# Kernel tuning notes

Hardware: AMD Instinct MI355X
Metric: run time of the kernel (lower is better)

Reference implementation:

```python
import jax, jax.numpy as jnp
import numpy as np

TEMP = 8.0      # config.router_temp
TOP_K = 2       # config.moe_top_k
EPS = 1e-8
LN_EPS = 1e-5


def _layer_norm_noaffine(x):
    # nn.LayerNorm(input_dim, elementwise_affine=False)
    mu = jnp.mean(x, axis=-1, keepdims=True)
    var = jnp.var(x, axis=-1, keepdims=True)
    return (x - mu) / jnp.sqrt(var + LN_EPS)


def _unit_norm(x):
    # x / x.norm(dim=-1).clamp(min=EPS)
    n = jnp.linalg.norm(x, axis=-1, keepdims=True)
    return x / jnp.maximum(n, EPS)


def setup_inputs() -> dict:
    key = jax.random.key(0)
    k1, k2 = jax.random.split(key)
    x = jax.random.normal(k1, (4, 4096, 2048), dtype=jnp.float32)
    prototypes = jax.random.normal(k2, (64, 2048), dtype=jnp.float32)
    return {"x": x, "prototypes": prototypes}


def reference(x, prototypes):
    # input_norm_fn = 'norm_d', proto_norm_fn = 'unit'
    xn = _layer_norm_noaffine(x)          # [b, s, d]
    pn = _unit_norm(prototypes)           # [e, d]
    logits = jnp.einsum('bsd,ed->bse', xn, pn) / TEMP   # [b, s, e]
    probs = jax.nn.softmax(logits, axis=-1)
    top_w, top_i = jax.lax.top_k(probs, TOP_K)          # [b, s, k]
    top_w = top_w / jnp.sum(top_w, axis=-1, keepdims=True)
    return top_w, top_i
```

## Files before the change

### kernel.cpp

```cpp
#include <hip/hip_runtime.h>
#include <math.h>

typedef __attribute__((ext_vector_type(8))) short short8;
typedef __attribute__((ext_vector_type(4))) float f32x4;

constexpr int kD  = 2048;
constexpr int kE  = 64;
constexpr int kM  = 16;
constexpr int kBK = 128;
constexpr int kIt = kD / kBK;
constexpr int kCS = 3136;

constexpr int kPlaneU = 4 * 64 * 512;
__device__ unsigned short g_B[3 * kPlaneU];

__device__ __forceinline__ void split3(float v, unsigned& h, unsigned& m, unsigned& l) {
  unsigned u = __float_as_uint(v);
  h = u & 0xFFFF0000u;
  float r1 = v - __uint_as_float(h);
  m = __float_as_uint(r1) & 0xFFFF0000u;
  float r2 = r1 - __uint_as_float(m);
  l = __float_as_uint(r2);
}

__device__ __forceinline__ void pack2(float e0, float e1,
                                      unsigned& dh, unsigned& dm, unsigned& dl) {
  unsigned h0, m0, l0, h1, m1, l1;
  split3(e0, h0, m0, l0);
  split3(e1, h1, m1, l1);
  dh = (h0 >> 16) | h1;
  dm = (m0 >> 16) | m1;
  dl = (l0 >> 16) | (l1 & 0xFFFF0000u);
}

__global__ __launch_bounds__(256) void proto_prep(const float* __restrict__ p,
                                                  float* __restrict__ ws) {
  const int e = blockIdx.x, t = threadIdx.x;
  const float* row = p + (size_t)e * kD;
  float4 v0 = *(const float4*)(row + 8 * t);
  float4 v1 = *(const float4*)(row + 8 * t + 4);

  unsigned dh[4], dm[4], dl[4];
  pack2(v0.x, v0.y, dh[0], dm[0], dl[0]);
  pack2(v0.z, v0.w, dh[1], dm[1], dl[1]);
  pack2(v1.x, v1.y, dh[2], dm[2], dl[2]);
  pack2(v1.z, v1.w, dh[3], dm[3], dl[3]);
  const int gc = t >> 2, o = t & 3;
  size_t base = (size_t)((e >> 4) * 64 + gc) * 512 + (16 * o + (e & 15)) * 8;
  *(uint4*)&g_B[base]               = make_uint4(dh[0], dh[1], dh[2], dh[3]);
  *(uint4*)&g_B[kPlaneU + base]     = make_uint4(dm[0], dm[1], dm[2], dm[3]);
  *(uint4*)&g_B[2 * kPlaneU + base] = make_uint4(dl[0], dl[1], dl[2], dl[3]);

  float s = (v0.x + v0.y) + (v0.z + v0.w) + (v1.x + v1.y) + (v1.z + v1.w);
  float q = v0.x*v0.x + v0.y*v0.y + v0.z*v0.z + v0.w*v0.w
          + v1.x*v1.x + v1.y*v1.y + v1.z*v1.z + v1.w*v1.w;
  #pragma unroll
  for (int off = 32; off >= 1; off >>= 1) {
    s += __shfl_xor(s, off, 64);
    q += __shfl_xor(q, off, 64);
  }
  __shared__ float as[4], aq[4];
  if ((t & 63) == 0) { as[t >> 6] = s; aq[t >> 6] = q; }
  __syncthreads();
  if (t == 0) {
    float S = (as[0] + as[1]) + (as[2] + as[3]);
    float Q = (aq[0] + aq[1]) + (aq[2] + aq[3]);
    ws[e]      = S;
    ws[kE + e] = 1.f / fmaxf(sqrtf(Q), 1e-8f);
  }
}

__global__ __launch_bounds__(256, 4) void router_main(
    const float* __restrict__ x, const float* __restrict__ ws,
    float* __restrict__ out_w, float* __restrict__ out_i) {
  __shared__ __align__(16) unsigned char sA[4 * kCS];
  __shared__ float sLogit[kM * 68];
  __shared__ float sStats[kM][2];

  const int t    = threadIdx.x;
  const int w    = t >> 6;
  const int L    = t & 63;
  const int ln15 = L & 15;
  const int q    = L >> 4;
  const int tok0 = blockIdx.x * kM;
  const float* xg = x + (size_t)tok0 * kD;

  f32x4 acc = (f32x4){0.f, 0.f, 0.f, 0.f};
  float sx[2] = {0.f, 0.f}, sxx[2] = {0.f, 0.f};

  float4 pf[2];
  #pragma unroll
  for (int jj = 0; jj < 2; ++jj) {
    int f = t + 256 * jj;
    pf[jj] = *(const float4*)(xg + (size_t)(f >> 5) * kD + (f & 31) * 4);
  }

  for (int it = 0; it < kIt; ++it) {
    __syncthreads();
    #pragma unroll
    for (int jj = 0; jj < 2; ++jj) {
      int f = t + 256 * jj;
      int c4 = f & 31, k = 4 * c4;
      int m = f >> 5, c = k >> 5, o = (k >> 3) & 3, j = k & 7;
      float4 v = pf[jj];
      sx[jj] += (v.x + v.y) + (v.z + v.w);
      sxx[jj] = fmaf(v.x, v.x, fmaf(v.y, v.y, fmaf(v.z, v.z, fmaf(v.w, v.w, sxx[jj]))));
      unsigned dh0, dm0, dl0, dh1, dm1, dl1;
      pack2(v.x, v.y, dh0, dm0, dl0);
      pack2(v.z, v.w, dh1, dm1, dl1);
      unsigned char* dst = sA + c * kCS + (16 * o + m) * 48 + o * 16 + j * 2;
      *(uint2*)(dst)      = make_uint2(dh0, dh1);
      *(uint2*)(dst + 16) = make_uint2(dm0, dm1);
      *(uint2*)(dst + 32) = make_uint2(dl0, dl1);
    }
    __syncthreads();
    if (it + 1 < kIt) {
      #pragma unroll
      for (int jj = 0; jj < 2; ++jj) {
        int f = t + 256 * jj;
        pf[jj] = *(const float4*)(xg + (size_t)(f >> 5) * kD + (it + 1) * kBK + (f & 31) * 4);
      }
    }
    #pragma unroll
    for (int c = 0; c < 4; ++c) {
      const int gc = it * 4 + c;
      const size_t bo = (size_t)(w * 64 + gc) * 512 + L * 8;
      short8 bh = *(const short8*)&g_B[bo];
      short8 bm = *(const short8*)&g_B[kPlaneU + bo];
      short8 bl = *(const short8*)&g_B[2 * kPlaneU + bo];
      const unsigned char* ra = sA + c * kCS + L * 48 + (L >> 4) * 16;
      short8 ah = *(const short8*)(ra);
      short8 am = *(const short8*)(ra + 16);
      short8 al = *(const short8*)(ra + 32);
      acc = __builtin_amdgcn_mfma_f32_16x16x32_bf16(ah, bh, acc, 0, 0, 0);
      acc = __builtin_amdgcn_mfma_f32_16x16x32_bf16(ah, bm, acc, 0, 0, 0);
      acc = __builtin_amdgcn_mfma_f32_16x16x32_bf16(am, bh, acc, 0, 0, 0);
      acc = __builtin_amdgcn_mfma_f32_16x16x32_bf16(am, bm, acc, 0, 0, 0);
      acc = __builtin_amdgcn_mfma_f32_16x16x32_bf16(ah, bl, acc, 0, 0, 0);
      acc = __builtin_amdgcn_mfma_f32_16x16x32_bf16(al, bh, acc, 0, 0, 0);
    }
  }

  #pragma unroll
  for (int jj = 0; jj < 2; ++jj) {
    float a = sx[jj], b = sxx[jj];
    #pragma unroll
    for (int off = 16; off >= 1; off >>= 1) {
      a += __shfl_xor(a, off, 64);
      b += __shfl_xor(b, off, 64);
    }
    if ((L & 31) == 0) {
      int m = (t >> 5) + 8 * jj;
      sStats[m][0] = a;
      sStats[m][1] = b;
    }
  }

  #pragma unroll
  for (int i = 0; i < 4; ++i)
    sLogit[(q * 4 + i) * 68 + w * 16 + ln15] = acc[i];
  __syncthreads();

  const float Se  = ws[L];
  const float inv = ws[kE + L];
  #pragma unroll
  for (int tl = 0; tl < 4; ++tl) {
    int tk = w * 4 + tl;
    float mu   = sStats[tk][0] * (1.f / kD);
    float var  = sStats[tk][1] * (1.f / kD) - mu * mu;
    float rstd = rsqrtf(var + 1e-5f);
    float logit = (sLogit[tk * 68 + L] - mu * Se) * rstd * inv * 0.125f;

    float v1 = logit; int i1 = L;
    #pragma unroll
    for (int off = 32; off >= 1; off >>= 1) {
      float ov = __shfl_xor(v1, off, 64);
      int   oi = __shfl_xor(i1, off, 64);
      if (ov > v1 || (ov == v1 && oi < i1)) { v1 = ov; i1 = oi; }
    }
    float ml = (L == i1) ? -3.402823466e38f : logit;
    float v2 = ml; int i2 = L;
    #pragma unroll
    for (int off = 32; off >= 1; off >>= 1) {
      float ov = __shfl_xor(v2, off, 64);
      int   oi = __shfl_xor(i2, off, 64);
      if (ov > v2 || (ov == v2 && oi < i2)) { v2 = ov; i2 = oi; }
    }
    if (L == 0) {
      int tg = tok0 + tk;
      float er = expf(v2 - v1);
      float r  = 1.f / (1.f + er);
      out_w[2 * tg]     = r;
      out_w[2 * tg + 1] = er * r;
      out_i[2 * tg]     = (float)i1;
      out_i[2 * tg + 1] = (float)i2;
    }
  }
}

extern "C" void kernel_launch(void* const* d_in, const int* in_sizes, int n_in,
                              void* d_out, int out_size, void* d_ws, size_t ws_size,
                              hipStream_t stream) {
  const float* x = (const float*)d_in[0];
  const float* p = (const float*)d_in[1];
  float* ws = (float*)d_ws;
  const int T = in_sizes[0] / kD;
  float* out_w = (float*)d_out;
  float* out_i = (float*)d_out + (size_t)T * 2;

  proto_prep<<<kE, 256, 0, stream>>>(p, ws);
  router_main<<<T / kM, 256, 0, stream>>>(x, ws, out_w, out_i);
}
```

Before: 226.7 us.

## Double-buffer A tiles, double tokens per block, software-pipeline B and A loads

Each block now handles 32 tokens instead of 16, so every loaded B fragment from the prototype planes feeds two MFMA accumulators. The shared A staging area is double-buffered, with x prefetched two iterations ahead and the next chunk's split and pack interleaved with the MFMAs, which leaves one barrier per iteration instead of two. B and A fragments for the next chunk are loaded before the current MFMAs issue. In exchange, shared memory and register use per block go up, launch bounds drop to 2 blocks per SM, and the grid has half as many blocks.

Measured after the change: 209.8 us. 1.08x faster.

```diff
diff --git a/kernel.cpp b/kernel.cpp
--- a/kernel.cpp
+++ b/kernel.cpp
@@ -6,10 +6,12 @@
 
 constexpr int kD  = 2048;
 constexpr int kE  = 64;
-constexpr int kM  = 16;
+constexpr int kM  = 32;
 constexpr int kBK = 128;
 constexpr int kIt = kD / kBK;
-constexpr int kCS = 3136;
+constexpr int kTS  = 3136;
+constexpr int kCS2 = 2 * kTS;
+constexpr int kBuf = 4 * kCS2;
 
 constexpr int kPlaneU = 4 * 64 * 512;
 __device__ unsigned short g_B[3 * kPlaneU];
@@ -70,10 +72,10 @@
   }
 }
 
-__global__ __launch_bounds__(256, 4) void router_main(
+__global__ __launch_bounds__(256, 2) void router_main(
     const float* __restrict__ x, const float* __restrict__ ws,
     float* __restrict__ out_w, float* __restrict__ out_i) {
-  __shared__ __align__(16) unsigned char sA[4 * kCS];
+  __shared__ __align__(16) unsigned char sA[2 * kBuf];
   __shared__ float sLogit[kM * 68];
   __shared__ float sStats[kM][2];
 
@@ -85,64 +87,122 @@
   const int tok0 = blockIdx.x * kM;
   const float* xg = x + (size_t)tok0 * kD;
 
-  f32x4 acc = (f32x4){0.f, 0.f, 0.f, 0.f};
-  float sx[2] = {0.f, 0.f}, sxx[2] = {0.f, 0.f};
-
-  float4 pf[2];
-  #pragma unroll
-  for (int jj = 0; jj < 2; ++jj) {
-    int f = t + 256 * jj;
-    pf[jj] = *(const float4*)(xg + (size_t)(f >> 5) * kD + (f & 31) * 4);
-  }
+  const int mB = t >> 5;
+  const int kc = (t & 31) * 4;
+  const int c_s = kc >> 5;
+  const int o_s = (kc >> 3) & 3;
+  const int j_s = kc & 7;
+  const int wcol = (16 * o_s) * 48 + o_s * 16 + j_s * 2;
+
+  f32x4 acc0 = (f32x4){0.f, 0.f, 0.f, 0.f};
+  f32x4 acc1 = (f32x4){0.f, 0.f, 0.f, 0.f};
+  float sx[4]  = {0.f, 0.f, 0.f, 0.f};
+  float sxx[4] = {0.f, 0.f, 0.f, 0.f};
+
+  auto stage = [&](const float4 v, float& sxr, float& sxxr, int m, unsigned char* wb) {
+    unsigned dh0, dm0, dl0, dh1, dm1, dl1;
+    pack2(v.x, v.y, dh0, dm0, dl0);
+    pack2(v.z, v.w, dh1, dm1, dl1);
+    sxr += (v.x + v.y) + (v.z + v.w);
+    sxxr = fmaf(v.x, v.x, fmaf(v.y, v.y, fmaf(v.z, v.z, fmaf(v.w, v.w, sxxr))));
+    unsigned char* dst = wb + c_s * kCS2 + (m >> 4) * kTS + (m & 15) * 48 + wcol;
+    *(uint2*)(dst)      = make_uint2(dh0, dh1);
+    *(uint2*)(dst + 16) = make_uint2(dm0, dm1);
+    *(uint2*)(dst + 32) = make_uint2(dl0, dl1);
+  };
+
+  float4 pfA[4], pfB[4];
+  #pragma unroll
+  for (int jj = 0; jj < 4; ++jj)
+    pfA[jj] = *(const float4*)(xg + (size_t)(mB + 8 * jj) * kD + kc);
+  #pragma unroll
+  for (int jj = 0; jj < 4; ++jj)
+    stage(pfA[jj], sx[jj], sxx[jj], mB + 8 * jj, sA);
+  #pragma unroll
+  for (int jj = 0; jj < 4; ++jj)
+    pfA[jj] = *(const float4*)(xg + (size_t)(mB + 8 * jj) * kD + kBK + kc);
+
+  short8 Bh, Bm, Bl;
+  {
+    const size_t bo = (size_t)(w * 64) * 512 + L * 8;
+    Bh = *(const short8*)&g_B[bo];
+    Bm = *(const short8*)&g_B[kPlaneU + bo];
+    Bl = *(const short8*)&g_B[2 * kPlaneU + bo];
+  }
+  __syncthreads();
+
+  const int aoff = L * 48 + (L >> 4) * 16;
 
   for (int it = 0; it < kIt; ++it) {
+    unsigned char* rbase = sA + (it & 1) * kBuf;
+    unsigned char* wbase = sA + ((it & 1) ^ 1) * kBuf;
+
+    if (it + 2 < kIt) {
+      #pragma unroll
+      for (int jj = 0; jj < 4; ++jj)
+        pfB[jj] = *(const float4*)(xg + (size_t)(mB + 8 * jj) * kD + (it + 2) * kBK + kc);
+    }
+
+    const unsigned char* ra = rbase + aoff;
+    short8 Ah0 = *(const short8*)(ra);
+    short8 Am0 = *(const short8*)(ra + 16);
+    short8 Al0 = *(const short8*)(ra + 32);
+    short8 Ah1 = *(const short8*)(ra + kTS);
+    short8 Am1 = *(const short8*)(ra + kTS + 16);
+    short8 Al1 = *(const short8*)(ra + kTS + 32);
+
+    const bool do_stage = (it + 1 < kIt);
+
+    #pragma unroll
+    for (int c = 0; c < 4; ++c) {
+      const int ngc = (it * 4 + c + 1) & 63;
+      const size_t nbo = (size_t)(w * 64 + ngc) * 512 + L * 8;
+      short8 nBh = *(const short8*)&g_B[nbo];
+      short8 nBm = *(const short8*)&g_B[kPlaneU + nbo];
+      short8 nBl = *(const short8*)&g_B[2 * kPlaneU + nbo];
+
+      short8 nAh0 = Ah0, nAm0 = Am0, nAl0 = Al0;
+      short8 nAh1 = Ah1, nAm1 = Am1, nAl1 = Al1;
+      if (c < 3) {
+        const unsigned char* rn = rbase + (c + 1) * kCS2 + aoff;
+        nAh0 = *(const short8*)(rn);
+        nAm0 = *(const short8*)(rn + 16);
+        nAl0 = *(const short8*)(rn + 32);
+        nAh1 = *(const short8*)(rn + kTS);
+        nAm1 = *(const short8*)(rn + kTS + 16);
+        nAl1 = *(const short8*)(rn + kTS + 32);
+      }
+
+      acc0 = __builtin_amdgcn_mfma_f32_16x16x32_bf16(Ah0, Bh, acc0, 0, 0, 0);
+      acc1 = __builtin_amdgcn_mfma_f32_16x16x32_bf16(Ah1, Bh, acc1, 0, 0, 0);
+      acc0 = __builtin_amdgcn_mfma_f32_16x16x32_bf16(Ah0, Bm, acc0, 0, 0, 0);
+      acc1 = __builtin_amdgcn_mfma_f32_16x16x32_bf16(Ah1, Bm, acc1, 0, 0, 0);
+      acc0 = __builtin_amdgcn_mfma_f32_16x16x32_bf16(Am0, Bh, acc0, 0, 0, 0);
+      acc1 = __builtin_amdgcn_mfma_f32_16x16x32_bf16(Am1, Bh, acc1, 0, 0, 0);
+      acc0 = __builtin_amdgcn_mfma_f32_16x16x32_bf16(Am0, Bm, acc0, 0, 0, 0);
+      acc1 = __builtin_amdgcn_mfma_f32_16x16x32_bf16(Am1, Bm, acc1, 0, 0, 0);
+      acc0 = __builtin_amdgcn_mfma_f32_16x16x32_bf16(Ah0, Bl, acc0, 0, 0, 0);
+      acc1 = __builtin_amdgcn_mfma_f32_16x16x32_bf16(Ah1, Bl, acc1, 0, 0, 0);
+      acc0 = __builtin_amdgcn_mfma_f32_16x16x32_bf16(Al0, Bh, acc0, 0, 0, 0);
+      acc1 = __builtin_amdgcn_mfma_f32_16x16x32_bf16(Al1, Bh, acc1, 0, 0, 0);
+
+      if (do_stage)
+        stage(pfA[c], sx[c], sxx[c], mB + 8 * c, wbase);
+
+      Bh = nBh; Bm = nBm; Bl = nBl;
+      Ah0 = nAh0; Am0 = nAm0; Al0 = nAl0;
+      Ah1 = nAh1; Am1 = nAm1; Al1 = nAl1;
+    }
+
     __syncthreads();
-    #pragma unroll
-    for (int jj = 0; jj < 2; ++jj) {
-      int f = t + 256 * jj;
-      int c4 = f & 31, k = 4 * c4;
-      int m = f >> 5, c = k >> 5, o = (k >> 3) & 3, j = k & 7;
-      float4 v = pf[jj];
-      sx[jj] += (v.x + v.y) + (v.z + v.w);
-      sxx[jj] = fmaf(v.x, v.x, fmaf(v.y, v.y, fmaf(v.z, v.z, fmaf(v.w, v.w, sxx[jj]))));
-      unsigned dh0, dm0, dl0, dh1, dm1, dl1;
-      pack2(v.x, v.y, dh0, dm0, dl0);
-      pack2(v.z, v.w, dh1, dm1, dl1);
-      unsigned char* dst = sA + c * kCS + (16 * o + m) * 48 + o * 16 + j * 2;
-      *(uint2*)(dst)      = make_uint2(dh0, dh1);
-      *(uint2*)(dst + 16) = make_uint2(dm0, dm1);
-      *(uint2*)(dst + 32) = make_uint2(dl0, dl1);
-    }
-    __syncthreads();
-    if (it + 1 < kIt) {
+    if (it + 2 < kIt) {
       #pragma unroll
-      for (int jj = 0; jj < 2; ++jj) {
-        int f = t + 256 * jj;
-        pf[jj] = *(const float4*)(xg + (size_t)(f >> 5) * kD + (it + 1) * kBK + (f & 31) * 4);
-      }
-    }
-    #pragma unroll
-    for (int c = 0; c < 4; ++c) {
-      const int gc = it * 4 + c;
-      const size_t bo = (size_t)(w * 64 + gc) * 512 + L * 8;
-      short8 bh = *(const short8*)&g_B[bo];
-      short8 bm = *(const short8*)&g_B[kPlaneU + bo];
-      short8 bl = *(const short8*)&g_B[2 * kPlaneU + bo];
-      const unsigned char* ra = sA + c * kCS + L * 48 + (L >> 4) * 16;
-      short8 ah = *(const short8*)(ra);
-      short8 am = *(const short8*)(ra + 16);
-      short8 al = *(const short8*)(ra + 32);
-      acc = __builtin_amdgcn_mfma_f32_16x16x32_bf16(ah, bh, acc, 0, 0, 0);
-      acc = __builtin_amdgcn_mfma_f32_16x16x32_bf16(ah, bm, acc, 0, 0, 0);
-      acc = __builtin_amdgcn_mfma_f32_16x16x32_bf16(am, bh, acc, 0, 0, 0);
-      acc = __builtin_amdgcn_mfma_f32_16x16x32_bf16(am, bm, acc, 0, 0, 0);
-      acc = __builtin_amdgcn_mfma_f32_16x16x32_bf16(ah, bl, acc, 0, 0, 0);
-      acc = __builtin_amdgcn_mfma_f32_16x16x32_bf16(al, bh, acc, 0, 0, 0);
-    }
-  }
-
-  #pragma unroll
-  for (int jj = 0; jj < 2; ++jj) {
+      for (int jj = 0; jj < 4; ++jj) pfA[jj] = pfB[jj];
+    }
+  }
+
+  #pragma unroll
+  for (int jj = 0; jj < 4; ++jj) {
     float a = sx[jj], b = sxx[jj];
     #pragma unroll
     for (int off = 16; off >= 1; off >>= 1) {
@@ -150,22 +210,24 @@
       b += __shfl_xor(b, off, 64);
     }
     if ((L & 31) == 0) {
-      int m = (t >> 5) + 8 * jj;
+      int m = mB + 8 * jj;
       sStats[m][0] = a;
       sStats[m][1] = b;
     }
   }
 
   #pragma unroll
-  for (int i = 0; i < 4; ++i)
-    sLogit[(q * 4 + i) * 68 + w * 16 + ln15] = acc[i];
+  for (int i = 0; i < 4; ++i) {
+    sLogit[(q * 4 + i) * 68 + w * 16 + ln15]      = acc0[i];
+    sLogit[(16 + q * 4 + i) * 68 + w * 16 + ln15] = acc1[i];
+  }
   __syncthreads();
 
   const float Se  = ws[L];
   const float inv = ws[kE + L];
   #pragma unroll
-  for (int tl = 0; tl < 4; ++tl) {
-    int tk = w * 4 + tl;
+  for (int tl = 0; tl < 8; ++tl) {
+    int tk = w * 8 + tl;
     float mu   = sStats[tk][0] * (1.f / kD);
     float var  = sStats[tk][1] * (1.f / kD) - mu * mu;
     float rstd = rsqrtf(var + 1e-5f);
```

## Double-buffer LDS staging, prefetch x two tiles ahead, widen block to 32 tokens

Applied to the files above, without the earlier changes.

Restructures the router GEMM loop into a double-buffered LDS pipeline with a single barrier per iteration. x is prefetched into registers two K-tiles ahead, and prototype fragments are prefetched one chunk ahead. Blocks now hold 32 tokens across 8 waves (two token halves times four expert groups) with a K tile of 64, and MFMA groups are wrapped in s_setprio to favour matrix issue. This aims to hide global and LDS latency behind MFMA work, at the cost of more registers and LDS per block, which may reduce occupancy.

Result: faster. 217.9 us (-3.9%).

```diff
diff --git a/kernel.cpp b/kernel.cpp
--- a/kernel.cpp
+++ b/kernel.cpp
@@ -6,10 +6,12 @@
 
 constexpr int kD  = 2048;
 constexpr int kE  = 64;
-constexpr int kM  = 16;
-constexpr int kBK = 128;
+constexpr int kM  = 32;
+constexpr int kBK = 64;
 constexpr int kIt = kD / kBK;
-constexpr int kCS = 3136;
+constexpr int kTS  = 3136;
+constexpr int kCS2 = 2 * kTS;
+constexpr int kBuf = 2 * kCS2;
 
 constexpr int kPlaneU = 4 * 64 * 512;
 __device__ unsigned short g_B[3 * kPlaneU];
@@ -70,87 +72,128 @@
   }
 }
 
-__global__ __launch_bounds__(256, 4) void router_main(
+__global__ __launch_bounds__(512, 4) void router_main(
     const float* __restrict__ x, const float* __restrict__ ws,
     float* __restrict__ out_w, float* __restrict__ out_i) {
-  __shared__ __align__(16) unsigned char sA[4 * kCS];
+  __shared__ __align__(16) unsigned char sA[2 * kBuf];
   __shared__ float sLogit[kM * 68];
   __shared__ float sStats[kM][2];
 
   const int t    = threadIdx.x;
   const int w    = t >> 6;
   const int L    = t & 63;
+  const int eg   = w & 3;
+  const int th   = w >> 2;
   const int ln15 = L & 15;
   const int q    = L >> 4;
   const int tok0 = blockIdx.x * kM;
   const float* xg = x + (size_t)tok0 * kD;
 
+  const int mS   = t >> 4;
+  const int colS = (t & 15) * 4;
+  const int cS   = colS >> 5;
+  const int oS   = (colS >> 3) & 3;
+  const int jS   = colS & 7;
+  const int woff = cS * kCS2 + (mS >> 4) * kTS + (mS & 15) * 48
+                 + (16 * oS) * 48 + oS * 16 + jS * 2;
+
   f32x4 acc = (f32x4){0.f, 0.f, 0.f, 0.f};
-  float sx[2] = {0.f, 0.f}, sxx[2] = {0.f, 0.f};
-
-  float4 pf[2];
-  #pragma unroll
-  for (int jj = 0; jj < 2; ++jj) {
-    int f = t + 256 * jj;
-    pf[jj] = *(const float4*)(xg + (size_t)(f >> 5) * kD + (f & 31) * 4);
-  }
+  float sx = 0.f, sxx = 0.f;
+
+  auto stage = [&](const float4 v, unsigned char* wb) {
+    unsigned dh0, dm0, dl0, dh1, dm1, dl1;
+    pack2(v.x, v.y, dh0, dm0, dl0);
+    pack2(v.z, v.w, dh1, dm1, dl1);
+    sx += (v.x + v.y) + (v.z + v.w);
+    sxx = fmaf(v.x, v.x, fmaf(v.y, v.y, fmaf(v.z, v.z, fmaf(v.w, v.w, sxx))));
+    unsigned char* dst = wb + woff;
+    *(uint2*)(dst)      = make_uint2(dh0, dh1);
+    *(uint2*)(dst + 16) = make_uint2(dm0, dm1);
+    *(uint2*)(dst + 32) = make_uint2(dl0, dl1);
+  };
+
+  float4 pfA, pfB;
+  pfA = *(const float4*)(xg + (size_t)mS * kD + colS);
+  stage(pfA, sA);
+  pfA = *(const float4*)(xg + (size_t)mS * kD + kBK + colS);
+  pfB = pfA;
+
+  short8 Bch, Bcm, Bcl;
+  {
+    const size_t bo = (size_t)(eg * 64 + 0) * 512 + L * 8;
+    Bch = *(const short8*)&g_B[bo];
+    Bcm = *(const short8*)&g_B[kPlaneU + bo];
+    Bcl = *(const short8*)&g_B[2 * kPlaneU + bo];
+  }
+  __syncthreads();
+
+  const int aoff = th * kTS + L * 48 + (L >> 4) * 16;
 
   for (int it = 0; it < kIt; ++it) {
+    unsigned char* rb = sA + (it & 1) * kBuf;
+    unsigned char* wb = sA + ((it & 1) ^ 1) * kBuf;
+
+    if (it + 2 < kIt)
+      pfB = *(const float4*)(xg + (size_t)mS * kD + (it + 2) * kBK + colS);
+
+    const unsigned char* ra0 = rb + aoff;
+    short8 Ah0 = *(const short8*)(ra0);
+    short8 Am0 = *(const short8*)(ra0 + 16);
+    short8 Al0 = *(const short8*)(ra0 + 32);
+
+    const int gc1 = it * 2 + 1;
+    const size_t bo1 = (size_t)(eg * 64 + gc1) * 512 + L * 8;
+    short8 Bnh = *(const short8*)&g_B[bo1];
+    short8 Bnm = *(const short8*)&g_B[kPlaneU + bo1];
+    short8 Bnl = *(const short8*)&g_B[2 * kPlaneU + bo1];
+
+    if (it + 1 < kIt)
+      stage(pfA, wb);
+
+    const unsigned char* ra1 = rb + kCS2 + aoff;
+    short8 Ah1 = *(const short8*)(ra1);
+    short8 Am1 = *(const short8*)(ra1 + 16);
+    short8 Al1 = *(const short8*)(ra1 + 32);
+
+    __builtin_amdgcn_s_setprio(1);
+    acc = __builtin_amdgcn_mfma_f32_16x16x32_bf16(Ah0, Bch, acc, 0, 0, 0);
+    acc = __builtin_amdgcn_mfma_f32_16x16x32_bf16(Ah0, Bcm, acc, 0, 0, 0);
+    acc = __builtin_amdgcn_mfma_f32_16x16x32_bf16(Am0, Bch, acc, 0, 0, 0);
+    acc = __builtin_amdgcn_mfma_f32_16x16x32_bf16(Am0, Bcm, acc, 0, 0, 0);
+    acc = __builtin_amdgcn_mfma_f32_16x16x32_bf16(Ah0, Bcl, acc, 0, 0, 0);
+    acc = __builtin_amdgcn_mfma_f32_16x16x32_bf16(Al0, Bch, acc, 0, 0, 0);
+    __builtin_amdgcn_s_setprio(0);
+
+    const int gc2 = (it * 2 + 2) & 63;
+    const size_t bo2 = (size_t)(eg * 64 + gc2) * 512 + L * 8;
+    short8 Bfh = *(const short8*)&g_B[bo2];
+    short8 Bfm = *(const short8*)&g_B[kPlaneU + bo2];
+    short8 Bfl = *(const short8*)&g_B[2 * kPlaneU + bo2];
+
+    __builtin_amdgcn_s_setprio(1);
+    acc = __builtin_amdgcn_mfma_f32_16x16x32_bf16(Ah1, Bnh, acc, 0, 0, 0);
+    acc = __builtin_amdgcn_mfma_f32_16x16x32_bf16(Ah1, Bnm, acc, 0, 0, 0);
+    acc = __builtin_amdgcn_mfma_f32_16x16x32_bf16(Am1, Bnh, acc, 0, 0, 0);
+    acc = __builtin_amdgcn_mfma_f32_16x16x32_bf16(Am1, Bnm, acc, 0, 0, 0);
+    acc = __builtin_amdgcn_mfma_f32_16x16x32_bf16(Ah1, Bnl, acc, 0, 0, 0);
+    acc = __builtin_amdgcn_mfma_f32_16x16x32_bf16(Al1, Bnh, acc, 0, 0, 0);
+    __builtin_amdgcn_s_setprio(0);
+
+    Bch = Bfh; Bcm = Bfm; Bcl = Bfl;
+
     __syncthreads();
+    if (it + 2 < kIt) pfA = pfB;
+  }
+
+  {
+    float a = sx, b = sxx;
     #pragma unroll
-    for (int jj = 0; jj < 2; ++jj) {
-      int f = t + 256 * jj;
-      int c4 = f & 31, k = 4 * c4;
-      int m = f >> 5, c = k >> 5, o = (k >> 3) & 3, j = k & 7;
-      float4 v = pf[jj];
-      sx[jj] += (v.x + v.y) + (v.z + v.w);
-      sxx[jj] = fmaf(v.x, v.x, fmaf(v.y, v.y, fmaf(v.z, v.z, fmaf(v.w, v.w, sxx[jj]))));
-      unsigned dh0, dm0, dl0, dh1, dm1, dl1;
-      pack2(v.x, v.y, dh0, dm0, dl0);
-      pack2(v.z, v.w, dh1, dm1, dl1);
-      unsigned char* dst = sA + c * kCS + (16 * o + m) * 48 + o * 16 + j * 2;
-      *(uint2*)(dst)      = make_uint2(dh0, dh1);
-      *(uint2*)(dst + 16) = make_uint2(dm0, dm1);
-      *(uint2*)(dst + 32) = make_uint2(dl0, dl1);
-    }
-    __syncthreads();
-    if (it + 1 < kIt) {
-      #pragma unroll
-      for (int jj = 0; jj < 2; ++jj) {
-        int f = t + 256 * jj;
-        pf[jj] = *(const float4*)(xg + (size_t)(f >> 5) * kD + (it + 1) * kBK + (f & 31) * 4);
-      }
-    }
-    #pragma unroll
-    for (int c = 0; c < 4; ++c) {
-      const int gc = it * 4 + c;
-      const size_t bo = (size_t)(w * 64 + gc) * 512 + L * 8;
-      short8 bh = *(const short8*)&g_B[bo];
-      short8 bm = *(const short8*)&g_B[kPlaneU + bo];
-      short8 bl = *(const short8*)&g_B[2 * kPlaneU + bo];
-      const unsigned char* ra = sA + c * kCS + L * 48 + (L >> 4) * 16;
-      short8 ah = *(const short8*)(ra);
-      short8 am = *(const short8*)(ra + 16);
-      short8 al = *(const short8*)(ra + 32);
-      acc = __builtin_amdgcn_mfma_f32_16x16x32_bf16(ah, bh, acc, 0, 0, 0);
-      acc = __builtin_amdgcn_mfma_f32_16x16x32_bf16(ah, bm, acc, 0, 0, 0);
-      acc = __builtin_amdgcn_mfma_f32_16x16x32_bf16(am, bh, acc, 0, 0, 0);
-      acc = __builtin_amdgcn_mfma_f32_16x16x32_bf16(am, bm, acc, 0, 0, 0);
-      acc = __builtin_amdgcn_mfma_f32_16x16x32_bf16(ah, bl, acc, 0, 0, 0);
-      acc = __builtin_amdgcn_mfma_f32_16x16x32_bf16(al, bh, acc, 0, 0, 0);
-    }
-  }
-
-  #pragma unroll
-  for (int jj = 0; jj < 2; ++jj) {
-    float a = sx[jj], b = sxx[jj];
-    #pragma unroll
-    for (int off = 16; off >= 1; off >>= 1) {
+    for (int off = 8; off >= 1; off >>= 1) {
       a += __shfl_xor(a, off, 64);
       b += __shfl_xor(b, off, 64);
     }
-    if ((L & 31) == 0) {
-      int m = (t >> 5) + 8 * jj;
+    if ((L & 15) == 0) {
+      int m = 4 * w + (L >> 4);
       sStats[m][0] = a;
       sStats[m][1] = b;
     }
@@ -158,7 +201,7 @@
 
   #pragma unroll
   for (int i = 0; i < 4; ++i)
-    sLogit[(q * 4 + i) * 68 + w * 16 + ln15] = acc[i];
+    sLogit[(th * 16 + q * 4 + i) * 68 + eg * 16 + ln15] = acc[i];
   __syncthreads();
 
   const float Se  = ws[L];
@@ -209,5 +252,5 @@
   float* out_i = (float*)d_out + (size_t)T * 2;
 
   proto_prep<<<kE, 256, 0, stream>>>(p, ws);
-  router_main<<<T / kM, 256, 0, stream>>>(x, ws, out_w, out_i);
-}
+  router_main<<<T / kM, 512, 0, stream>>>(x, ws, out_w, out_i);
+}
```

## Restructure router GEMM with async global-to-LDS triple buffering and 32x32 MFMA

Applied to the files above, without the earlier changes.

The main kernel now processes 64 tokens per block with 512 threads. It stages raw fp32 x tiles into a triple-buffered, XOR-swizzled LDS ring through global_load_lds, and splits them into bf16 hi/mid/lo fragments in registers instead of in a separate LDS packing pass. The GEMM uses 32x32x16 MFMAs with two accumulators, split-K across wave pairs, and register-prefetched prototype fragments under one barrier per iteration, which is meant to cut LDS traffic, barriers and global latency stalls. The cost is a larger shared-memory footprint, hand-placed vmcnt waits that must match the load counts exactly, and an extra reduction step for split-K partial logits and statistics.

New measurement: 222.5 us. No clear change (-1.8%).

```diff
diff --git a/kernel.cpp b/kernel.cpp
--- a/kernel.cpp
+++ b/kernel.cpp
@@ -1,18 +1,24 @@
 #include <hip/hip_runtime.h>
 #include <math.h>
 
-typedef __attribute__((ext_vector_type(8))) short short8;
-typedef __attribute__((ext_vector_type(4))) float f32x4;
+typedef __attribute__((ext_vector_type(8)))  short short8;
+typedef __attribute__((ext_vector_type(16))) float f32x16;
 
 constexpr int kD  = 2048;
 constexpr int kE  = 64;
-constexpr int kM  = 16;
-constexpr int kBK = 128;
+constexpr int kM  = 64;
+constexpr int kBK = 64;
 constexpr int kIt = kD / kBK;
-constexpr int kCS = 3136;
-
-constexpr int kPlaneU = 4 * 64 * 512;
+
+constexpr int kXBuf = 64 * 256;
+
+constexpr int kPlaneU = 2 * 64 * 2 * 64 * 8;
 __device__ unsigned short g_B[3 * kPlaneU];
+
+#define GLOAD_LDS16(gp, lp)                                                   \
+  __builtin_amdgcn_global_load_lds(                                          \
+      (const __attribute__((address_space(1))) unsigned int*)(gp),           \
+      (__attribute__((address_space(3))) unsigned int*)(lp), 16, 0, 0)
 
 __device__ __forceinline__ void split3(float v, unsigned& h, unsigned& m, unsigned& l) {
   unsigned u = __float_as_uint(v);
@@ -33,6 +39,19 @@
   dl = (l0 >> 16) | (l1 & 0xFFFF0000u);
 }
 
+__device__ __forceinline__ void mk_frag(float4 va, float4 vb,
+                                        short8& Ah, short8& Am, short8& Al) {
+  unsigned h0,m0,l0,h1,m1,l1,h2,m2,l2,h3,m3,l3;
+  pack2(va.x, va.y, h0, m0, l0);
+  pack2(va.z, va.w, h1, m1, l1);
+  pack2(vb.x, vb.y, h2, m2, l2);
+  pack2(vb.z, vb.w, h3, m3, l3);
+  union { unsigned u[4]; short8 s; } U;
+  U.u[0]=h0; U.u[1]=h1; U.u[2]=h2; U.u[3]=h3; Ah = U.s;
+  U.u[0]=m0; U.u[1]=m1; U.u[2]=m2; U.u[3]=m3; Am = U.s;
+  U.u[0]=l0; U.u[1]=l1; U.u[2]=l2; U.u[3]=l3; Al = U.s;
+}
+
 __global__ __launch_bounds__(256) void proto_prep(const float* __restrict__ p,
                                                   float* __restrict__ ws) {
   const int e = blockIdx.x, t = threadIdx.x;
@@ -45,8 +64,11 @@
   pack2(v0.z, v0.w, dh[1], dm[1], dl[1]);
   pack2(v1.x, v1.y, dh[2], dm[2], dl[2]);
   pack2(v1.z, v1.w, dh[3], dm[3], dl[3]);
-  const int gc = t >> 2, o = t & 3;
-  size_t base = (size_t)((e >> 4) * 64 + gc) * 512 + (16 * o + (e & 15)) * 8;
+  const int gc = t >> 2;
+  const int kh = (t >> 1) & 1;
+  const int lb = t & 1;
+  size_t base = ((((size_t)(e >> 5) * 64 + gc) * 2 + kh) * 64
+                 + ((e & 31) | (lb << 5))) * 8;
   *(uint4*)&g_B[base]               = make_uint4(dh[0], dh[1], dh[2], dh[3]);
   *(uint4*)&g_B[kPlaneU + base]     = make_uint4(dm[0], dm[1], dm[2], dm[3]);
   *(uint4*)&g_B[2 * kPlaneU + base] = make_uint4(dl[0], dl[1], dl[2], dl[3]);
@@ -70,104 +92,164 @@
   }
 }
 
-__global__ __launch_bounds__(256, 4) void router_main(
+__global__ __launch_bounds__(512, 2) void router_main(
     const float* __restrict__ x, const float* __restrict__ ws,
     float* __restrict__ out_w, float* __restrict__ out_i) {
-  __shared__ __align__(16) unsigned char sA[4 * kCS];
-  __shared__ float sLogit[kM * 68];
-  __shared__ float sStats[kM][2];
+  __shared__ __align__(16) unsigned char sA[3 * kXBuf];
 
   const int t    = threadIdx.x;
   const int w    = t >> 6;
   const int L    = t & 63;
-  const int ln15 = L & 15;
-  const int q    = L >> 4;
+  const int tt   = w >> 2;
+  const int eg   = (w >> 1) & 1;
+  const int kp   = w & 1;
   const int tok0 = blockIdx.x * kM;
   const float* xg = x + (size_t)tok0 * kD;
 
-  f32x4 acc = (f32x4){0.f, 0.f, 0.f, 0.f};
-  float sx[2] = {0.f, 0.f}, sxx[2] = {0.f, 0.f};
-
-  float4 pf[2];
+  auto stageIt = [&](int its, int bufI) {
+    unsigned char* base = sA + bufI * kXBuf;
+    const int kbase = its * kBK;
+    #pragma unroll
+    for (int qq = 0; qq < 2; ++qq) {
+      const int r0  = w * 8 + qq * 4;
+      const int row = r0 + (L >> 4);
+      const int slot = (L & 15) ^ (row & 15);
+      const float* gp = xg + (size_t)row * kD + kbase + slot * 4;
+      unsigned char* lp = base + r0 * 256 + L * 16;
+      GLOAD_LDS16(gp, lp);
+    }
+  };
+
+  auto bIdx = [&](int g, int kh) -> size_t {
+    return ((((size_t)eg * 64 + g) * 2 + kh) * 64 + L) * 8;
+  };
+
+  f32x16 accA, accB;
   #pragma unroll
-  for (int jj = 0; jj < 2; ++jj) {
-    int f = t + 256 * jj;
-    pf[jj] = *(const float4*)(xg + (size_t)(f >> 5) * kD + (f & 31) * 4);
-  }
+  for (int i = 0; i < 16; ++i) { accA[i] = 0.f; accB[i] = 0.f; }
+  float sx = 0.f, sxx = 0.f;
+
+  stageIt(0, 0);
+  stageIt(1, 1);
+  short8 BcH0, BcM0, BcL0, BcH1, BcM1, BcL1;
+  {
+    size_t b0 = bIdx(kp, 0), b1 = bIdx(kp, 1);
+    BcH0 = *(const short8*)&g_B[b0];
+    BcM0 = *(const short8*)&g_B[kPlaneU + b0];
+    BcL0 = *(const short8*)&g_B[2 * kPlaneU + b0];
+    BcH1 = *(const short8*)&g_B[b1];
+    BcM1 = *(const short8*)&g_B[kPlaneU + b1];
+    BcL1 = *(const short8*)&g_B[2 * kPlaneU + b1];
+  }
+
+  const int aRow  = tt * 32 + (L & 31);
+  const unsigned char* rRow0 = sA + aRow * 256;
+  const int sw    = aRow & 15;
+  const int sBase = kp * 8 + 2 * (L >> 5);
 
   for (int it = 0; it < kIt; ++it) {
-    __syncthreads();
-    #pragma unroll
-    for (int jj = 0; jj < 2; ++jj) {
-      int f = t + 256 * jj;
-      int c4 = f & 31, k = 4 * c4;
-      int m = f >> 5, c = k >> 5, o = (k >> 3) & 3, j = k & 7;
-      float4 v = pf[jj];
-      sx[jj] += (v.x + v.y) + (v.z + v.w);
-      sxx[jj] = fmaf(v.x, v.x, fmaf(v.y, v.y, fmaf(v.z, v.z, fmaf(v.w, v.w, sxx[jj]))));
-      unsigned dh0, dm0, dl0, dh1, dm1, dl1;
-      pack2(v.x, v.y, dh0, dm0, dl0);
-      pack2(v.z, v.w, dh1, dm1, dl1);
-      unsigned char* dst = sA + c * kCS + (16 * o + m) * 48 + o * 16 + j * 2;
-      *(uint2*)(dst)      = make_uint2(dh0, dh1);
-      *(uint2*)(dst + 16) = make_uint2(dm0, dm1);
-      *(uint2*)(dst + 32) = make_uint2(dl0, dl1);
-    }
-    __syncthreads();
+    short8 BnH0 = BcH0, BnM0 = BcM0, BnL0 = BcL0;
+    short8 BnH1 = BcH1, BnM1 = BcM1, BnL1 = BcL1;
     if (it + 1 < kIt) {
-      #pragma unroll
-      for (int jj = 0; jj < 2; ++jj) {
-        int f = t + 256 * jj;
-        pf[jj] = *(const float4*)(xg + (size_t)(f >> 5) * kD + (it + 1) * kBK + (f & 31) * 4);
-      }
-    }
-    #pragma unroll
-    for (int c = 0; c < 4; ++c) {
-      const int gc = it * 4 + c;
-      const size_t bo = (size_t)(w * 64 + gc) * 512 + L * 8;
-      short8 bh = *(const short8*)&g_B[bo];
-      short8 bm = *(const short8*)&g_B[kPlaneU + bo];
-      short8 bl = *(const short8*)&g_B[2 * kPlaneU + bo];
-      const unsigned char* ra = sA + c * kCS + L * 48 + (L >> 4) * 16;
-      short8 ah = *(const short8*)(ra);
-      short8 am = *(const short8*)(ra + 16);
-      short8 al = *(const short8*)(ra + 32);
-      acc = __builtin_amdgcn_mfma_f32_16x16x32_bf16(ah, bh, acc, 0, 0, 0);
-      acc = __builtin_amdgcn_mfma_f32_16x16x32_bf16(ah, bm, acc, 0, 0, 0);
-      acc = __builtin_amdgcn_mfma_f32_16x16x32_bf16(am, bh, acc, 0, 0, 0);
-      acc = __builtin_amdgcn_mfma_f32_16x16x32_bf16(am, bm, acc, 0, 0, 0);
-      acc = __builtin_amdgcn_mfma_f32_16x16x32_bf16(ah, bl, acc, 0, 0, 0);
-      acc = __builtin_amdgcn_mfma_f32_16x16x32_bf16(al, bh, acc, 0, 0, 0);
-    }
-  }
-
-  #pragma unroll
-  for (int jj = 0; jj < 2; ++jj) {
-    float a = sx[jj], b = sxx[jj];
-    #pragma unroll
-    for (int off = 16; off >= 1; off >>= 1) {
-      a += __shfl_xor(a, off, 64);
-      b += __shfl_xor(b, off, 64);
-    }
-    if ((L & 31) == 0) {
-      int m = (t >> 5) + 8 * jj;
-      sStats[m][0] = a;
-      sStats[m][1] = b;
-    }
-  }
-
-  #pragma unroll
-  for (int i = 0; i < 4; ++i)
-    sLogit[(q * 4 + i) * 68 + w * 16 + ln15] = acc[i];
+      const int g1 = 2 * (it + 1) + kp;
+      size_t b0 = bIdx(g1, 0), b1 = bIdx(g1, 1);
+      BnH0 = *(const short8*)&g_B[b0];
+      BnM0 = *(const short8*)&g_B[kPlaneU + b0];
+      BnL0 = *(const short8*)&g_B[2 * kPlaneU + b0];
+      BnH1 = *(const short8*)&g_B[b1];
+      BnM1 = *(const short8*)&g_B[kPlaneU + b1];
+      BnL1 = *(const short8*)&g_B[2 * kPlaneU + b1];
+    }
+
+    if (it + 1 < kIt) asm volatile("s_waitcnt vmcnt(14)" ::: "memory");
+    else              asm volatile("s_waitcnt vmcnt(6)"  ::: "memory");
+    __builtin_amdgcn_sched_barrier(0);
+
+    __builtin_amdgcn_s_barrier();
+    __builtin_amdgcn_sched_barrier(0);
+
+    if (it + 2 < kIt) stageIt(it + 2, (it + 2) % 3);
+
+    const unsigned char* rb = rRow0 + (it % 3) * kXBuf;
+    float4 va0 = *(const float4*)(rb + (((sBase    )     ) ^ sw) * 16);
+    float4 vb0 = *(const float4*)(rb + (((sBase    ) + 1 ) ^ sw) * 16);
+    float4 va1 = *(const float4*)(rb + (((sBase + 4)     ) ^ sw) * 16);
+    float4 vb1 = *(const float4*)(rb + (((sBase + 4) + 1 ) ^ sw) * 16);
+
+    if (eg == 0) {
+      sx  += ((va0.x + va0.y) + (va0.z + va0.w)) + ((vb0.x + vb0.y) + (vb0.z + vb0.w))
+           + ((va1.x + va1.y) + (va1.z + va1.w)) + ((vb1.x + vb1.y) + (vb1.z + vb1.w));
+      float q0 = fmaf(va0.x,va0.x, fmaf(va0.y,va0.y, fmaf(va0.z,va0.z, va0.w*va0.w)));
+      float q1 = fmaf(vb0.x,vb0.x, fmaf(vb0.y,vb0.y, fmaf(vb0.z,vb0.z, vb0.w*vb0.w)));
+      float q2 = fmaf(va1.x,va1.x, fmaf(va1.y,va1.y, fmaf(va1.z,va1.z, va1.w*va1.w)));
+      float q3 = fmaf(vb1.x,vb1.x, fmaf(vb1.y,vb1.y, fmaf(vb1.z,vb1.z, vb1.w*vb1.w)));
+      sxx += (q0 + q1) + (q2 + q3);
+    }
+
+    short8 Ah0, Am0, Al0, Ah1, Am1, Al1;
+    mk_frag(va0, vb0, Ah0, Am0, Al0);
+    mk_frag(va1, vb1, Ah1, Am1, Al1);
+
+    __builtin_amdgcn_s_setprio(1);
+    accA = __builtin_amdgcn_mfma_f32_32x32x16_bf16(Ah0, BcH0, accA, 0, 0, 0);
+    accB = __builtin_amdgcn_mfma_f32_32x32x16_bf16(Ah1, BcH1, accB, 0, 0, 0);
+    accA = __builtin_amdgcn_mfma_f32_32x32x16_bf16(Ah0, BcM0, accA, 0, 0, 0);
+    accB = __builtin_amdgcn_mfma_f32_32x32x16_bf16(Ah1, BcM1, accB, 0, 0, 0);
+    accA = __builtin_amdgcn_mfma_f32_32x32x16_bf16(Am0, BcH0, accA, 0, 0, 0);
+    accB = __builtin_amdgcn_mfma_f32_32x32x16_bf16(Am1, BcH1, accB, 0, 0, 0);
+    accA = __builtin_amdgcn_mfma_f32_32x32x16_bf16(Am0, BcM0, accA, 0, 0, 0);
+    accB = __builtin_amdgcn_mfma_f32_32x32x16_bf16(Am1, BcM1, accB, 0, 0, 0);
+    accA = __builtin_amdgcn_mfma_f32_32x32x16_bf16(Ah0, BcL0, accA, 0, 0, 0);
+    accB = __builtin_amdgcn_mfma_f32_32x32x16_bf16(Ah1, BcL1, accB, 0, 0, 0);
+    accA = __builtin_amdgcn_mfma_f32_32x32x16_bf16(Al0, BcH0, accA, 0, 0, 0);
+    accB = __builtin_amdgcn_mfma_f32_32x32x16_bf16(Al1, BcH1, accB, 0, 0, 0);
+    __builtin_amdgcn_s_setprio(0);
+
+    BcH0 = BnH0; BcM0 = BnM0; BcL0 = BnL0;
+    BcH1 = BnH1; BcM1 = BnM1; BcL1 = BnL1;
+  }
+
+  __syncthreads();
+
+  float* sLogit  = (float*)sA;
+  float* sStatsP = (float*)(sA + kM * 68 * 4);
+
+  if (eg == 0) {
+    float a = sx  + __shfl_xor(sx, 32, 64);
+    float b = sxx + __shfl_xor(sxx, 32, 64);
+    if (L < 32) {
+      int m = tt * 32 + L;
+      sStatsP[(kp * kM + m) * 2 + 0] = a;
+      sStatsP[(kp * kM + m) * 2 + 1] = b;
+    }
+  }
+
+  if (kp == 0) {
+    #pragma unroll
+    for (int i = 0; i < 16; ++i) {
+      int row = (i & 3) + 8 * (i >> 2) + 4 * (L >> 5);
+      sLogit[(tt * 32 + row) * 68 + eg * 32 + (L & 31)] = accA[i] + accB[i];
+    }
+  }
+  __syncthreads();
+  if (kp == 1) {
+    #pragma unroll
+    for (int i = 0; i < 16; ++i) {
+      int row = (i & 3) + 8 * (i >> 2) + 4 * (L >> 5);
+      sLogit[(tt * 32 + row) * 68 + eg * 32 + (L & 31)] += accA[i] + accB[i];
+    }
+  }
   __syncthreads();
 
   const float Se  = ws[L];
   const float inv = ws[kE + L];
   #pragma unroll
-  for (int tl = 0; tl < 4; ++tl) {
-    int tk = w * 4 + tl;
-    float mu   = sStats[tk][0] * (1.f / kD);
-    float var  = sStats[tk][1] * (1.f / kD) - mu * mu;
+  for (int tl = 0; tl < 8; ++tl) {
+    int tk = w * 8 + tl;
+    float st0 = sStatsP[tk * 2 + 0] + sStatsP[(kM + tk) * 2 + 0];
+    float st1 = sStatsP[tk * 2 + 1] + sStatsP[(kM + tk) * 2 + 1];
+    float mu   = st0 * (1.f / kD);
+    float var  = st1 * (1.f / kD) - mu * mu;
     float rstd = rsqrtf(var + 1e-5f);
     float logit = (sLogit[tk * 68 + L] - mu * Se) * rstd * inv * 0.125f;
 
@@ -209,5 +291,5 @@
   float* out_i = (float*)d_out + (size_t)T * 2;
 
   proto_prep<<<kE, 256, 0, stream>>>(p, ws);
-  router_main<<<T / kM, 256, 0, stream>>>(x, ws, out_w, out_i);
-}
+  router_main<<<T / kM, 512, 0, stream>>>(x, ws, out_w, out_i);
+}
```
